# Performance work log

Hardware: AMD Instinct MI355X
Metric: run time of the kernel (lower is better)

Reference implementation:

```python
import jax, jax.numpy as jnp
import numpy as np

MAX_VAL = 10000.0
KS = (1, 5, 10, 20, 50)
B, V, L = 256, 128000, 200


def setup_inputs() -> dict:
    key = jax.random.key(0)
    k1, k2, k3 = jax.random.split(key, 3)
    scores = jax.random.normal(k1, (B, V), dtype=jnp.float32)
    labels = jax.random.randint(k2, (B,), 0, V, dtype=jnp.int64)
    seqs = jax.random.randint(k3, (B, L), 0, V, dtype=jnp.int64)
    return {"scores": scores, "labels": labels, "seqs": seqs}


def reference(scores, labels, seqs):
    b = scores.shape[0]
    rows = jnp.arange(b)
    # gather predicted score for the true label BEFORE masking (torch order)
    predicts = scores[rows, labels]  # [B]
    # scatter -MAX_VAL at history items (masked scatter)
    masked = scores.at[rows[:, None], seqs].set(-MAX_VAL)  # [B, V]
    valid_length = (masked > -MAX_VAL).sum(-1).astype(jnp.float32)  # [B]
    rank = (predicts[:, None] < masked).sum(-1).astype(jnp.float32)  # [B]
    res = []
    for k in KS:
        indicator = (rank < k).astype(jnp.float32)
        res.append((indicator / jnp.log2(rank + 2.0)).mean())  # NDCG@k
        res.append(indicator.mean())  # Recall@k
    res.append((1.0 / (rank + 1.0)).mean())  # MRR
    res.append((1.0 - rank / valid_length).mean())  # AUC-like
    res.append(jnp.float32(0.0))
    return jnp.stack(res)
```

## Files before the change

kernel.cpp:

```cpp
#include <hip/hip_runtime.h>
#include <math.h>

#define B_CONST 256
#define V_CONST 128000
#define L_CONST 200
#define SLICES  25
#define F4_PER_SLICE 1280
#define F4_PER_LANE  20

typedef float f32x4 __attribute__((ext_vector_type(4)));


__global__ __launch_bounds__(128, 4) void rank_count_kernel(
    const float* __restrict__ scores,
    const int* __restrict__ labels,
    const int* __restrict__ seqs,
    int* __restrict__ partial,
    int* __restrict__ sub,
    int* __restrict__ dist)
{
    const int lane = threadIdx.x & 63;
    const int b    = blockIdx.y;
    const int t    = blockIdx.x * 2 + (threadIdx.x >> 6);

    const float* row = scores + (size_t)b * V_CONST;

    const float predict = row[labels[b]];

    if (t < SLICES) {
        const f32x4* row4 = (const f32x4*)row;
        const int base = t * F4_PER_SLICE + lane;
        f32x4 v[F4_PER_LANE];
        #pragma unroll
        for (int k = 0; k < F4_PER_LANE; ++k)
            v[k] = __builtin_nontemporal_load(row4 + base + k * 64);

        int cnt = 0;
        #pragma unroll
        for (int k = 0; k < F4_PER_LANE; ++k) {
            cnt += __popcll(__ballot(v[k][0] > predict));
            cnt += __popcll(__ballot(v[k][1] > predict));
            cnt += __popcll(__ballot(v[k][2] > predict));
            cnt += __popcll(__ballot(v[k][3] > predict));
        }
        if (lane == 0) partial[t * B_CONST + b] = cnt;
    } else {
        const int* sq = seqs + b * L_CONST;
        int e[4], val[4];
        float sv[4];
        #pragma unroll
        for (int k = 0; k < 4; ++k) {
            e[k]   = lane + 64 * k;
            val[k] = (e[k] < L_CONST) ? sq[e[k]] : -1;
            sv[k]  = (e[k] < L_CONST) ? row[val[k]] : -1.0e30f;
        }
        bool first[4] = {true, true, true, true};
        #pragma unroll
        for (int jb = 0; jb < 4; ++jb) {
            for (int l = 0; l < 64; ++l) {
                const int j  = jb * 64 + l;
                const int sj = __shfl(val[jb], l);
                #pragma unroll
                for (int k = jb; k < 4; ++k)
                    if (j < e[k] && sj == val[k]) first[k] = false;
            }
        }
        int d = 0, s = 0;
        #pragma unroll
        for (int k = 0; k < 4; ++k) {
            const bool isdist = first[k] && (e[k] < L_CONST);
            d += __popcll(__ballot(isdist));
            s += __popcll(__ballot(isdist && (sv[k] > predict)));
        }
        if (lane == 0) { dist[b] = d; sub[b] = s; }
    }
}

__global__ __launch_bounds__(64) void finalize_kernel(
    const int* __restrict__ partial,
    const int* __restrict__ sub,
    const int* __restrict__ dist,
    float* __restrict__ out)
{
    const int l = threadIdx.x;

    float acc[12];
    #pragma unroll
    for (int q = 0; q < 12; ++q) acc[q] = 0.0f;

    const float ks[5] = {1.0f, 5.0f, 10.0f, 20.0f, 50.0f};

    #pragma unroll
    for (int r = 0; r < 4; ++r) {
        const int b = l + 64 * r;
        int gt = 0;
        #pragma unroll
        for (int s = 0; s < SLICES; ++s) gt += partial[s * B_CONST + b];
        const float rank  = (float)(gt - sub[b]);
        const float valid = (float)(V_CONST - dist[b]);

        const float invlog = 1.0f / log2f(rank + 2.0f);
        #pragma unroll
        for (int i = 0; i < 5; ++i) {
            const float ind = (rank < ks[i]) ? 1.0f : 0.0f;
            acc[2 * i]     += ind * invlog;
            acc[2 * i + 1] += ind;
        }
        acc[10] += 1.0f / (rank + 1.0f);
        acc[11] += 1.0f - rank / valid;
    }

    #pragma unroll
    for (int q = 0; q < 12; ++q) {
        float v = acc[q];
        #pragma unroll
        for (int off = 32; off > 0; off >>= 1)
            v += __shfl_down(v, off, 64);
        if (l == 0) out[q] = v * (1.0f / B_CONST);
    }
    if (l == 0) out[12] = 0.0f;
}

extern "C" void kernel_launch(void* const* d_in, const int* in_sizes, int n_in,
                              void* d_out, int out_size, void* d_ws, size_t ws_size,
                              hipStream_t stream) {
    const float* scores = (const float*)d_in[0];
    const int*   labels = (const int*)d_in[1];
    const int*   seqs   = (const int*)d_in[2];
    float* out = (float*)d_out;
    int*   ws  = (int*)d_ws;

    int* partial = ws;
    int* sub     = ws + SLICES * B_CONST;
    int* dist    = ws + SLICES * B_CONST + B_CONST;

    rank_count_kernel<<<dim3(13, B_CONST), 128, 0, stream>>>(
        scores, labels, seqs, partial, sub, dist);
    finalize_kernel<<<1, 64, 0, stream>>>(partial, sub, dist, out);
}
```

Baseline: 195.9 us.

## Restructure rank count into 8 waves per row with double-buffered loads

Each row is now split across 8 waves in two 256-thread blocks, and each wave streams 4000 float4s. It uses a double-buffered register pipeline (A/Bv, 8 float4s each) so loads overlap the ballot counting, where before each wave loaded 20 float4s in one burst. The history dedup work moves into wave 0 of each row instead of a separate dedicated wave, so it runs after that wave's streaming. The aim is to cut block count and per-block overhead and to keep more loads in flight. The cost is that wave 0 does extra serial work, which may lengthen the tail.

```diff
diff --git a/kernel.cpp b/kernel.cpp
--- a/kernel.cpp
+++ b/kernel.cpp
@@ -4,82 +4,124 @@
 #define B_CONST 256
 #define V_CONST 128000
 #define L_CONST 200
-#define SLICES  25
-#define F4_PER_SLICE 1280
-#define F4_PER_LANE  20
+#define F4_PER_ROW 32000
+#define F4_PER_WAVE 4000
+#define WPR 8
 
 typedef float f32x4 __attribute__((ext_vector_type(4)));
 
 
-__global__ __launch_bounds__(128, 4) void rank_count_kernel(
+__device__ __forceinline__ int cnt4(const f32x4 v, const float p) {
+    int c = 0;
+    c += __popcll(__ballot(v[0] > p));
+    c += __popcll(__ballot(v[1] > p));
+    c += __popcll(__ballot(v[2] > p));
+    c += __popcll(__ballot(v[3] > p));
+    return c;
+}
+
+__global__ __launch_bounds__(256) void rank_count_kernel(
     const float* __restrict__ scores,
     const int* __restrict__ labels,
     const int* __restrict__ seqs,
     int* __restrict__ partial,
-    int* __restrict__ sub,
-    int* __restrict__ dist)
+    int* __restrict__ subv,
+    int* __restrict__ distv)
 {
-    const int lane = threadIdx.x & 63;
-    const int b    = blockIdx.y;
-    const int t    = blockIdx.x * 2 + (threadIdx.x >> 6);
+    const int tid  = threadIdx.x;
+    const int lane = tid & 63;
+    const int w    = tid >> 6;
+    const int b    = blockIdx.x >> 1;
+    const int t    = ((blockIdx.x & 1) << 2) + w;
 
     const float* row = scores + (size_t)b * V_CONST;
 
+    int   hval[4];
+    float hsv[4];
+    const bool histw = (t == 0);
+    if (histw) {
+        const int* sq = seqs + b * L_CONST;
+        #pragma unroll
+        for (int k = 0; k < 4; ++k) {
+            const int e = lane + 64 * k;
+            hval[k] = (e < L_CONST) ? sq[e] : -1;
+            hsv[k]  = (e < L_CONST) ? row[hval[k]] : 0.0f;
+        }
+    }
+
     const float predict = row[labels[b]];
 
-    if (t < SLICES) {
-        const f32x4* row4 = (const f32x4*)row;
-        const int base = t * F4_PER_SLICE + lane;
-        f32x4 v[F4_PER_LANE];
+    const f32x4* row4 = (const f32x4*)row;
+    const int base = t * F4_PER_WAVE + lane;
+
+    f32x4 A[8], Bv[8];
+    #pragma unroll
+    for (int j = 0; j < 8; ++j)
+        A[j] = __builtin_nontemporal_load(row4 + base + j * 64);
+
+    int cnt = 0;
+    #pragma unroll
+    for (int kb = 8; kb <= 40; kb += 16) {
         #pragma unroll
-        for (int k = 0; k < F4_PER_LANE; ++k)
-            v[k] = __builtin_nontemporal_load(row4 + base + k * 64);
+        for (int j = 0; j < 8; ++j)
+            Bv[j] = __builtin_nontemporal_load(row4 + base + (kb + j) * 64);
+        #pragma unroll
+        for (int j = 0; j < 8; ++j) cnt += cnt4(A[j], predict);
+        #pragma unroll
+        for (int j = 0; j < 8; ++j)
+            A[j] = __builtin_nontemporal_load(row4 + base + (kb + 8 + j) * 64);
+        #pragma unroll
+        for (int j = 0; j < 8; ++j) cnt += cnt4(Bv[j], predict);
+    }
+    #pragma unroll
+    for (int j = 0; j < 6; ++j)
+        Bv[j] = __builtin_nontemporal_load(row4 + base + (56 + j) * 64);
+    f32x4 tl = {0.0f, 0.0f, 0.0f, 0.0f};
+    if (lane < 32)
+        tl = __builtin_nontemporal_load(row4 + base + 62 * 64);
+    #pragma unroll
+    for (int j = 0; j < 8; ++j) cnt += cnt4(A[j], predict);
+    #pragma unroll
+    for (int j = 0; j < 6; ++j) cnt += cnt4(Bv[j], predict);
+    {
+        const bool m = lane < 32;
+        cnt += __popcll(__ballot(m && (tl[0] > predict)));
+        cnt += __popcll(__ballot(m && (tl[1] > predict)));
+        cnt += __popcll(__ballot(m && (tl[2] > predict)));
+        cnt += __popcll(__ballot(m && (tl[3] > predict)));
+    }
+    if (lane == 0) partial[b * WPR + t] = cnt;
 
-        int cnt = 0;
-        #pragma unroll
-        for (int k = 0; k < F4_PER_LANE; ++k) {
-            cnt += __popcll(__ballot(v[k][0] > predict));
-            cnt += __popcll(__ballot(v[k][1] > predict));
-            cnt += __popcll(__ballot(v[k][2] > predict));
-            cnt += __popcll(__ballot(v[k][3] > predict));
-        }
-        if (lane == 0) partial[t * B_CONST + b] = cnt;
-    } else {
-        const int* sq = seqs + b * L_CONST;
-        int e[4], val[4];
-        float sv[4];
-        #pragma unroll
-        for (int k = 0; k < 4; ++k) {
-            e[k]   = lane + 64 * k;
-            val[k] = (e[k] < L_CONST) ? sq[e[k]] : -1;
-            sv[k]  = (e[k] < L_CONST) ? row[val[k]] : -1.0e30f;
-        }
+    if (histw) {
         bool first[4] = {true, true, true, true};
         #pragma unroll
         for (int jb = 0; jb < 4; ++jb) {
             for (int l = 0; l < 64; ++l) {
                 const int j  = jb * 64 + l;
-                const int sj = __shfl(val[jb], l);
+                const int sj = __shfl(hval[jb], l);
                 #pragma unroll
-                for (int k = jb; k < 4; ++k)
-                    if (j < e[k] && sj == val[k]) first[k] = false;
+                for (int k = jb; k < 4; ++k) {
+                    const int e = lane + 64 * k;
+                    if (j < e && sj == hval[k]) first[k] = false;
+                }
             }
         }
         int d = 0, s = 0;
         #pragma unroll
         for (int k = 0; k < 4; ++k) {
-            const bool isdist = first[k] && (e[k] < L_CONST);
-            d += __popcll(__ballot(isdist));
-            s += __popcll(__ballot(isdist && (sv[k] > predict)));
+            const int  e   = lane + 64 * k;
+            const bool isd = first[k] && (e < L_CONST);
+            d += __popcll(__ballot(isd));
+            s += __popcll(__ballot(isd && (hsv[k] > predict)));
         }
-        if (lane == 0) { dist[b] = d; sub[b] = s; }
+        if (lane == 0) { distv[b] = d; subv[b] = s; }
     }
 }
 
 __global__ __launch_bounds__(64) void finalize_kernel(
     const int* __restrict__ partial,
-    const int* __restrict__ sub,
-    const int* __restrict__ dist,
+    const int* __restrict__ subv,
+    const int* __restrict__ distv,
     float* __restrict__ out)
 {
     const int l = threadIdx.x;
@@ -95,9 +137,9 @@
         const int b = l + 64 * r;
         int gt = 0;
         #pragma unroll
-        for (int s = 0; s < SLICES; ++s) gt += partial[s * B_CONST + b];
-        const float rank  = (float)(gt - sub[b]);
-        const float valid = (float)(V_CONST - dist[b]);
+        for (int s = 0; s < WPR; ++s) gt += partial[b * WPR + s];
+        const float rank  = (float)(gt - subv[b]);
+        const float valid = (float)(V_CONST - distv[b]);
 
         const float invlog = 1.0f / log2f(rank + 2.0f);
         #pragma unroll
@@ -131,10 +173,10 @@
     int*   ws  = (int*)d_ws;
 
     int* partial = ws;
-    int* sub     = ws + SLICES * B_CONST;
-    int* dist    = ws + SLICES * B_CONST + B_CONST;
+    int* subv    = ws + B_CONST * WPR;
+    int* distv   = ws + B_CONST * WPR + B_CONST;
 
-    rank_count_kernel<<<dim3(13, B_CONST), 128, 0, stream>>>(
-        scores, labels, seqs, partial, sub, dist);
-    finalize_kernel<<<1, 64, 0, stream>>>(partial, sub, dist, out);
+    rank_count_kernel<<<dim3(2 * B_CONST), 256, 0, stream>>>(
+        scores, labels, seqs, partial, subv, distv);
+    finalize_kernel<<<1, 64, 0, stream>>>(partial, subv, distv, out);
 }
```

After: 199.6 us. About the same (+1.9%).
